# Kernel tuning notes

Measured on AMD Instinct MI355X. Metric: run time of the kernel, lower is better.

## Reference

```python
import jax, jax.numpy as jnp
import numpy as np

FILTER_SIZE = 7
SIGMA = 1.5
K1 = 0.01
K2 = 0.03
MAX_VAL = 1.0
CHANNEL = 1


def _gaussian_kernel3d(size, channel, sigma):
    coords = jnp.arange(size, dtype=jnp.float32) - (size - 1.0) / 2.0
    g = -(coords ** 2) / (2.0 * sigma ** 2)
    # grid[i,j,k] = g[j] + g[i] + g[k], matching torch view(1,-1,1)+view(-1,1,1)+view(1,1,-1)
    grid = g[None, :, None] + g[:, None, None] + g[None, None, :]
    grid = jax.nn.softmax(grid.reshape(-1))
    kernel = grid.reshape(1, 1, size, size, size)
    return jnp.broadcast_to(kernel, (channel, 1, size, size, size))


def _dwconv3d(x, kernel, channel):
    # depthwise (groups=channel) valid conv, NCDHW
    return jax.lax.conv_general_dilated(
        x, kernel, window_strides=(1, 1, 1), padding='VALID',
        dimension_numbers=('NCDHW', 'OIDHW', 'NCDHW'),
        feature_group_count=channel)


def setup_inputs() -> dict:
    key = jax.random.key(0)
    k1, k2 = jax.random.split(key)
    shape = (2, 1, 192, 192, 192)
    return {
        'input': jax.random.uniform(k1, shape, dtype=jnp.float32),
        'target': jax.random.uniform(k2, shape, dtype=jnp.float32),
    }


def reference(input, target):
    kernel = _gaussian_kernel3d(FILTER_SIZE, CHANNEL, SIGMA)
    c1 = (K1 * MAX_VAL) ** 2
    c2 = (K2 * MAX_VAL) ** 2
    mu1 = _dwconv3d(input, kernel, CHANNEL)
    mu2 = _dwconv3d(target, kernel, CHANNEL)
    mu1_sq = mu1 * mu1
    mu2_sq = mu2 * mu2
    mu1_mu2 = mu1 * mu2
    sigma1_sq = _dwconv3d(input * input, kernel, CHANNEL) - mu1_sq
    sigma2_sq = _dwconv3d(target * target, kernel, CHANNEL) - mu2_sq
    sigma12 = _dwconv3d(input * target, kernel, CHANNEL) - mu1_mu2
    v1 = 2.0 * sigma12 + c2
    v2 = sigma1_sq + sigma2_sq + c2
    ssim = (2.0 * mu1_mu2 + c1) * v1 / ((mu1_sq + mu2_sq + c1) * v2)
    return jnp.mean(ssim)  # reduction='mean'
```

## Files before the change

kernel.cpp:

```cpp
#include <hip/hip_runtime.h>
#include <utility>


#define DIMS 192
#define OD   186
#define VOL  (DIMS * DIMS * DIMS)
#define ZCH  62
#define XCH  27
#define NCHX 7
#define NP   (XCH + 6)
#define YT   8
#define YIN  14

#define ZP_P   15
#define ZP_F   (ZCH * ZP_P)
#define YP_F   576
#define YP_OFF (5 * ZP_F)
#define LDS_N  (YP_OFF + 5 * YP_F)

__global__ __launch_bounds__(256, 4)
void ssim3d_kernel(const float* __restrict__ X, const float* __restrict__ Y,
                   double* __restrict__ acc_out) {
    __shared__ float lds[LDS_N];
    __shared__ float wsum[4];
    const int tid = threadIdx.x;

    float w[7];
    {
        float s = 0.f;
        #pragma unroll
        for (int t = 0; t < 7; ++t) {
            float d = (float)t - 3.0f;
            w[t] = expf(-d * d / 4.5f);
            s += w[t];
        }
        #pragma unroll
        for (int t = 0; t < 7; ++t)
            w[t] = __uint_as_float(__builtin_amdgcn_readfirstlane(__float_as_uint(w[t] / s)));
    }

    const int z0 = blockIdx.x * ZCH;
    const int y0 = blockIdx.y * YT;
    const int cx = blockIdx.z % NCHX;
    const int n  = blockIdx.z / NCHX;
    const int x0 = cx * XCH;

    const float* Xb = X + (size_t)n * VOL;
    const float* Yb = Y + (size_t)n * VOL;

    const int zj = tid >> 4;
    const int zs = tid & 15;
    const bool zact = (zj < YIN);
    const int zc = z0 + zs * 4;
    const int gy = min(y0 + zj, DIMS - 1);
    const unsigned rowoff = (unsigned)gy * DIMS + (unsigned)zc;
    const bool ztail = (zc + 9 > DIMS - 1);

    const int wv = tid >> 6;
    const int ln = tid & 63;
    const int ybase = (310 * wv) >> 2;
    const int ycnt  = ((310 * (wv + 1)) >> 2) - ybase;

    const int aj = wv;
    const int ak = ln;
    const bool v1 = (ak < ZCH) && (y0 + aj < OD);
    const bool v2 = (ak < ZCH) && (y0 + aj + 4 < OD);
    const int xmax = OD + 6 - x0;

    float acc[7][10];
    #pragma unroll
    for (int q = 0; q < 7; ++q)
        #pragma unroll
        for (int m = 0; m < 10; ++m) acc[q][m] = 0.f;

    float lsum = 0.f;
    const float c1 = 1e-4f, c2 = 9e-4f;

    float pfx[10], pfy[10];

    auto loadX = [&](int xi) {
        if (!zact) return;
        int gx = min(x0 + xi, DIMS - 1);
        const float* p = Xb + (size_t)gx * (DIMS * DIMS) + rowoff;
        #pragma unroll
        for (int t = 0; t < 4; ++t) {
            float2 a = *(const float2*)(p + 2 * t);
            pfx[2 * t] = a.x; pfx[2 * t + 1] = a.y;
        }
        if (!ztail) {
            float2 a = *(const float2*)(p + 8);
            pfx[8] = a.x; pfx[9] = a.y;
        } else { pfx[8] = 0.f; pfx[9] = 0.f; }
    };
    auto loadY = [&](int xi) {
        if (!zact) return;
        int gx = min(x0 + xi, DIMS - 1);
        const float* p = Yb + (size_t)gx * (DIMS * DIMS) + rowoff;
        #pragma unroll
        for (int t = 0; t < 4; ++t) {
            float2 a = *(const float2*)(p + 2 * t);
            pfy[2 * t] = a.x; pfy[2 * t + 1] = a.y;
        }
        if (!ztail) {
            float2 a = *(const float2*)(p + 8);
            pfy[8] = a.x; pfy[9] = a.y;
        } else { pfy[8] = 0.f; pfy[9] = 0.f; }
    };

    auto ssim_pt = [&](float mu1, float mu2, float ex2, float ey2, float exy) {
        float mu11 = mu1 * mu1, mu22 = mu2 * mu2, mu12 = mu1 * mu2;
        float num = (2.f * mu12 + c1) * (2.f * (exy - mu12) + c2);
        float den = (mu11 + mu22 + c1) * ((ex2 - mu11) + (ey2 - mu22) + c2);
        lsum += num * __builtin_amdgcn_rcpf(den);
    };

    auto body = [&](int xi, auto ucell) {
        constexpr int U = decltype(ucell)::value;

        if (zact) {
            #pragma unroll
            for (int o = 0; o < 4; ++o) {
                float a0 = 0.f, a1 = 0.f, a2 = 0.f, a3 = 0.f, a4 = 0.f;
                #pragma unroll
                for (int t = 0; t < 7; ++t) {
                    float xx = pfx[o + t], yy = pfy[o + t], wt = w[t];
                    a0 += wt * xx;
                    a1 += wt * yy;
                    a2 += wt * (xx * xx);
                    a3 += wt * (yy * yy);
                    a4 += wt * (xx * yy);
                }
                int k = zs * 4 + o;
                if (k < ZCH) {
                    int b = k * ZP_P + zj;
                    lds[b]            = a0;
                    lds[b + ZP_F]     = a1;
                    lds[b + 2 * ZP_F] = a2;
                    lds[b + 3 * ZP_F] = a3;
                    lds[b + 4 * ZP_F] = a4;
                }
            }
        }
        if (xi + 1 < NP) loadX(xi + 1);
        __syncthreads();

        #pragma unroll
        for (int p2 = 0; p2 < 2; ++p2) {
            int rel = p2 * 64 + ln;
            if (rel < ycnt) {
                int t = ybase + rel;
                int f = t / ZCH;
                int k = t - f * ZCH;
                const float* src = &lds[f * ZP_F + k * ZP_P];
                float v[YIN];
                #pragma unroll
                for (int jj = 0; jj < YIN; ++jj) v[jj] = src[jj];
                float* dst = &lds[YP_OFF + f * YP_F + k * 9];
                #pragma unroll
                for (int j = 0; j < YT; ++j) {
                    float a = 0.f;
                    #pragma unroll
                    for (int tt = 0; tt < 7; ++tt) a += w[tt] * v[j + tt];
                    dst[j] = a;
                }
            }
        }
        if (xi + 1 < NP) loadY(xi + 1);
        __syncthreads();

        float vv[10];
        #pragma unroll
        for (int f = 0; f < 5; ++f) {
            vv[2 * f]     = lds[YP_OFF + f * YP_F + ak * 9 + aj];
            vv[2 * f + 1] = lds[YP_OFF + f * YP_F + ak * 9 + aj + 4];
        }
        #pragma unroll
        for (int d = 0; d < 7; ++d) {
            float wq = w[d];
            #pragma unroll
            for (int m = 0; m < 10; ++m)
                acc[(U + 7 - d) % 7][m] += wq * vv[m];
        }
        constexpr int sc = (U + 1) % 7;
        if (xi >= 6 && xi < xmax) {
            if (v1) ssim_pt(acc[sc][0], acc[sc][2], acc[sc][4], acc[sc][6], acc[sc][8]);
            if (v2) ssim_pt(acc[sc][1], acc[sc][3], acc[sc][5], acc[sc][7], acc[sc][9]);
        }
        #pragma unroll
        for (int m = 0; m < 10; ++m) acc[sc][m] = 0.f;
    };

    loadX(0); loadY(0);
    #pragma unroll 1
    for (int b = 0; b < 28; b += 7) {
        body(b + 0, std::integral_constant<int, 0>{});
        body(b + 1, std::integral_constant<int, 1>{});
        body(b + 2, std::integral_constant<int, 2>{});
        body(b + 3, std::integral_constant<int, 3>{});
        body(b + 4, std::integral_constant<int, 4>{});
        body(b + 5, std::integral_constant<int, 5>{});
        body(b + 6, std::integral_constant<int, 6>{});
    }
    body(28, std::integral_constant<int, 0>{});
    body(29, std::integral_constant<int, 1>{});
    body(30, std::integral_constant<int, 2>{});
    body(31, std::integral_constant<int, 3>{});
    body(32, std::integral_constant<int, 4>{});

    #pragma unroll
    for (int off = 32; off > 0; off >>= 1) lsum += __shfl_down(lsum, off, 64);
    if ((tid & 63) == 0) wsum[tid >> 6] = lsum;
    __syncthreads();
    if (tid == 0)
        atomicAdd(acc_out, (double)(wsum[0] + wsum[1] + wsum[2] + wsum[3]));
}

__global__ void ssim3d_finalize(const double* __restrict__ acc, float* __restrict__ out) {
    out[0] = (float)(acc[0] / 12869712.0);
}

extern "C" void kernel_launch(void* const* d_in, const int* in_sizes, int n_in,
                              void* d_out, int out_size, void* d_ws, size_t ws_size,
                              hipStream_t stream) {
    (void)in_sizes; (void)n_in; (void)out_size; (void)ws_size;
    const float* x = (const float*)d_in[0];
    const float* y = (const float*)d_in[1];
    float* out = (float*)d_out;
    double* acc = (double*)d_ws;
    hipMemsetAsync(d_ws, 0, sizeof(double), stream);
    dim3 grid(3, 24, NCHX * 2);
    ssim3d_kernel<<<grid, 256, 0, stream>>>(x, y, acc);
    ssim3d_finalize<<<1, 1, 0, stream>>>(acc, out);
}
```

Baseline: 235.8 us.

## Shrink z-tile to 32, double occupancy, remap blocks, fuse finalize via atomic counter

```diff
diff --git a/kernel.cpp b/kernel.cpp
--- a/kernel.cpp
+++ b/kernel.cpp
@@ -5,7 +5,8 @@
 #define DIMS 192
 #define OD   186
 #define VOL  (DIMS * DIMS * DIMS)
-#define ZCH  62
+#define ZCH  32
+#define NZT  6
 #define XCH  27
 #define NCHX 7
 #define NP   (XCH + 6)
@@ -14,13 +15,17 @@
 
 #define ZP_P   15
 #define ZP_F   (ZCH * ZP_P)
-#define YP_F   576
+#define YP_P   9
+#define YP_F   (ZCH * YP_P)
 #define YP_OFF (5 * ZP_F)
 #define LDS_N  (YP_OFF + 5 * YP_F)
 
-__global__ __launch_bounds__(256, 4)
+#define NBLK   (NZT * 24 * NCHX * 2)
+
+__global__ __launch_bounds__(256, 8)
 void ssim3d_kernel(const float* __restrict__ X, const float* __restrict__ Y,
-                   double* __restrict__ acc_out) {
+                   double* __restrict__ acc_out, unsigned* __restrict__ cnt,
+                   float* __restrict__ out) {
     __shared__ float lds[LDS_N];
     __shared__ float wsum[4];
     const int tid = threadIdx.x;
@@ -39,10 +44,17 @@
             w[t] = __uint_as_float(__builtin_amdgcn_readfirstlane(__float_as_uint(w[t] / s)));
     }
 
-    const int z0 = blockIdx.x * ZCH;
-    const int y0 = blockIdx.y * YT;
-    const int cx = blockIdx.z % NCHX;
-    const int n  = blockIdx.z / NCHX;
+    const int L  = blockIdx.x + NZT * (blockIdx.y + 24 * blockIdx.z);
+    const int v  = (L & 7) * (NBLK / 8) + (L >> 3);
+    const int cb = v / 144;
+    const int rem = v - cb * 144;
+    const int by  = rem % 24;
+    const int bz  = rem / 24;
+    const int cx  = cb % NCHX;
+    const int n   = cb / NCHX;
+
+    const int z0 = bz * ZCH;
+    const int y0 = by * YT;
     const int x0 = cx * XCH;
 
     const float* Xb = X + (size_t)n * VOL;
@@ -51,60 +63,66 @@
     const int zj = tid >> 4;
     const int zs = tid & 15;
     const bool zact = (zj < YIN);
-    const int zc = z0 + zs * 4;
+    const int zc = z0 + zs * 2;
     const int gy = min(y0 + zj, DIMS - 1);
     const unsigned rowoff = (unsigned)gy * DIMS + (unsigned)zc;
-    const bool ztail = (zc + 9 > DIMS - 1);
-
-    const int wv = tid >> 6;
-    const int ln = tid & 63;
-    const int ybase = (310 * wv) >> 2;
-    const int ycnt  = ((310 * (wv + 1)) >> 2) - ybase;
-
-    const int aj = wv;
-    const int ak = ln;
-    const bool v1 = (ak < ZCH) && (y0 + aj < OD);
-    const bool v2 = (ak < ZCH) && (y0 + aj + 4 < OD);
+    const bool ztail = (zc + 7 > DIMS - 1);
+
+    const int bfld = tid >> 5;
+    const int bk   = tid & 31;
+    const bool bact = (bfld < 5);
+
+    const int aj = tid >> 5;
+    const int ak = tid & 31;
+    const bool av = (z0 + ak < OD) && (y0 + aj < OD);
     const int xmax = OD + 6 - x0;
 
-    float acc[7][10];
+    float acc[7][5];
     #pragma unroll
     for (int q = 0; q < 7; ++q)
         #pragma unroll
-        for (int m = 0; m < 10; ++m) acc[q][m] = 0.f;
+        for (int m = 0; m < 5; ++m) acc[q][m] = 0.f;
 
     float lsum = 0.f;
     const float c1 = 1e-4f, c2 = 9e-4f;
 
-    float pfx[10], pfy[10];
+    float pfx[8], pfy[8];
 
     auto loadX = [&](int xi) {
         if (!zact) return;
         int gx = min(x0 + xi, DIMS - 1);
-        const float* p = Xb + (size_t)gx * (DIMS * DIMS) + rowoff;
-        #pragma unroll
-        for (int t = 0; t < 4; ++t) {
-            float2 a = *(const float2*)(p + 2 * t);
-            pfx[2 * t] = a.x; pfx[2 * t + 1] = a.y;
-        }
+        const float* p = Xb + (size_t)gx * (DIMS * DIMS);
         if (!ztail) {
-            float2 a = *(const float2*)(p + 8);
-            pfx[8] = a.x; pfx[9] = a.y;
-        } else { pfx[8] = 0.f; pfx[9] = 0.f; }
+            const float* q = p + rowoff;
+            #pragma unroll
+            for (int t = 0; t < 4; ++t) {
+                float2 a = *(const float2*)(q + 2 * t);
+                pfx[2 * t] = a.x; pfx[2 * t + 1] = a.y;
+            }
+        } else {
+            unsigned ro = (unsigned)gy * DIMS;
+            #pragma unroll
+            for (int j = 0; j < 8; ++j)
+                pfx[j] = p[ro + (unsigned)min(zc + j, DIMS - 1)];
+        }
     };
     auto loadY = [&](int xi) {
         if (!zact) return;
         int gx = min(x0 + xi, DIMS - 1);
-        const float* p = Yb + (size_t)gx * (DIMS * DIMS) + rowoff;
-        #pragma unroll
-        for (int t = 0; t < 4; ++t) {
-            float2 a = *(const float2*)(p + 2 * t);
-            pfy[2 * t] = a.x; pfy[2 * t + 1] = a.y;
-        }
+        const float* p = Yb + (size_t)gx * (DIMS * DIMS);
         if (!ztail) {
-            float2 a = *(const float2*)(p + 8);
-            pfy[8] = a.x; pfy[9] = a.y;
-        } else { pfy[8] = 0.f; pfy[9] = 0.f; }
+            const float* q = p + rowoff;
+            #pragma unroll
+            for (int t = 0; t < 4; ++t) {
+                float2 a = *(const float2*)(q + 2 * t);
+                pfy[2 * t] = a.x; pfy[2 * t + 1] = a.y;
+            }
+        } else {
+            unsigned ro = (unsigned)gy * DIMS;
+            #pragma unroll
+            for (int j = 0; j < 8; ++j)
+                pfy[j] = p[ro + (unsigned)min(zc + j, DIMS - 1)];
+        }
     };
 
     auto ssim_pt = [&](float mu1, float mu2, float ex2, float ey2, float exy) {
@@ -119,7 +137,7 @@
 
         if (zact) {
             #pragma unroll
-            for (int o = 0; o < 4; ++o) {
+            for (int o = 0; o < 2; ++o) {
                 float a0 = 0.f, a1 = 0.f, a2 = 0.f, a3 = 0.f, a4 = 0.f;
                 #pragma unroll
                 for (int t = 0; t < 7; ++t) {
@@ -130,64 +148,50 @@
                     a3 += wt * (yy * yy);
                     a4 += wt * (xx * yy);
                 }
-                int k = zs * 4 + o;
-                if (k < ZCH) {
-                    int b = k * ZP_P + zj;
-                    lds[b]            = a0;
-                    lds[b + ZP_F]     = a1;
-                    lds[b + 2 * ZP_F] = a2;
-                    lds[b + 3 * ZP_F] = a3;
-                    lds[b + 4 * ZP_F] = a4;
-                }
+                int b = (zs * 2 + o) * ZP_P + zj;
+                lds[b]            = a0;
+                lds[b + ZP_F]     = a1;
+                lds[b + 2 * ZP_F] = a2;
+                lds[b + 3 * ZP_F] = a3;
+                lds[b + 4 * ZP_F] = a4;
             }
         }
         if (xi + 1 < NP) loadX(xi + 1);
         __syncthreads();
 
-        #pragma unroll
-        for (int p2 = 0; p2 < 2; ++p2) {
-            int rel = p2 * 64 + ln;
-            if (rel < ycnt) {
-                int t = ybase + rel;
-                int f = t / ZCH;
-                int k = t - f * ZCH;
-                const float* src = &lds[f * ZP_F + k * ZP_P];
-                float v[YIN];
+        if (bact) {
+            const float* src = &lds[bfld * ZP_F + bk * ZP_P];
+            float vy[YIN];
+            #pragma unroll
+            for (int jj = 0; jj < YIN; ++jj) vy[jj] = src[jj];
+            float* dst = &lds[YP_OFF + bfld * YP_F + bk * YP_P];
+            #pragma unroll
+            for (int j = 0; j < YT; ++j) {
+                float a = 0.f;
                 #pragma unroll
-                for (int jj = 0; jj < YIN; ++jj) v[jj] = src[jj];
-                float* dst = &lds[YP_OFF + f * YP_F + k * 9];
-                #pragma unroll
-                for (int j = 0; j < YT; ++j) {
-                    float a = 0.f;
-                    #pragma unroll
-                    for (int tt = 0; tt < 7; ++tt) a += w[tt] * v[j + tt];
-                    dst[j] = a;
-                }
+                for (int tt = 0; tt < 7; ++tt) a += w[tt] * vy[j + tt];
+                dst[j] = a;
             }
         }
         if (xi + 1 < NP) loadY(xi + 1);
         __syncthreads();
 
-        float vv[10];
-        #pragma unroll
-        for (int f = 0; f < 5; ++f) {
-            vv[2 * f]     = lds[YP_OFF + f * YP_F + ak * 9 + aj];
-            vv[2 * f + 1] = lds[YP_OFF + f * YP_F + ak * 9 + aj + 4];
-        }
+        float vv[5];
+        #pragma unroll
+        for (int f = 0; f < 5; ++f)
+            vv[f] = lds[YP_OFF + f * YP_F + ak * YP_P + aj];
         #pragma unroll
         for (int d = 0; d < 7; ++d) {
             float wq = w[d];
             #pragma unroll
-            for (int m = 0; m < 10; ++m)
+            for (int m = 0; m < 5; ++m)
                 acc[(U + 7 - d) % 7][m] += wq * vv[m];
         }
         constexpr int sc = (U + 1) % 7;
-        if (xi >= 6 && xi < xmax) {
-            if (v1) ssim_pt(acc[sc][0], acc[sc][2], acc[sc][4], acc[sc][6], acc[sc][8]);
-            if (v2) ssim_pt(acc[sc][1], acc[sc][3], acc[sc][5], acc[sc][7], acc[sc][9]);
-        }
-        #pragma unroll
-        for (int m = 0; m < 10; ++m) acc[sc][m] = 0.f;
+        if (xi >= 6 && xi < xmax && av)
+            ssim_pt(acc[sc][0], acc[sc][1], acc[sc][2], acc[sc][3], acc[sc][4]);
+        #pragma unroll
+        for (int m = 0; m < 5; ++m) acc[sc][m] = 0.f;
     };
 
     loadX(0); loadY(0);
@@ -211,12 +215,16 @@
     for (int off = 32; off > 0; off >>= 1) lsum += __shfl_down(lsum, off, 64);
     if ((tid & 63) == 0) wsum[tid >> 6] = lsum;
     __syncthreads();
-    if (tid == 0)
-        atomicAdd(acc_out, (double)(wsum[0] + wsum[1] + wsum[2] + wsum[3]));
-}
-
-__global__ void ssim3d_finalize(const double* __restrict__ acc, float* __restrict__ out) {
-    out[0] = (float)(acc[0] / 12869712.0);
+    if (tid == 0) {
+        double bs = (double)(wsum[0] + wsum[1] + wsum[2] + wsum[3]);
+        atomicAdd(acc_out, bs);
+        __threadfence();
+        unsigned prev = atomicAdd(cnt, 1u);
+        if (prev == (unsigned)(NBLK - 1)) {
+            double tot = atomicAdd(acc_out, 0.0);
+            out[0] = (float)(tot / 12869712.0);
+        }
+    }
 }
 
 extern "C" void kernel_launch(void* const* d_in, const int* in_sizes, int n_in,
@@ -225,10 +233,9 @@
     (void)in_sizes; (void)n_in; (void)out_size; (void)ws_size;
     const float* x = (const float*)d_in[0];
     const float* y = (const float*)d_in[1];
-    float* out = (float*)d_out;
     double* acc = (double*)d_ws;
-    hipMemsetAsync(d_ws, 0, sizeof(double), stream);
-    dim3 grid(3, 24, NCHX * 2);
-    ssim3d_kernel<<<grid, 256, 0, stream>>>(x, y, acc);
-    ssim3d_finalize<<<1, 1, 0, stream>>>(acc, out);
+    unsigned* cnt = (unsigned*)((char*)d_ws + 8);
+    hipMemsetAsync(d_ws, 0, 16, stream);
+    dim3 grid(NZT, 24, NCHX * 2);
+    ssim3d_kernel<<<grid, 256, 0, stream>>>(x, y, acc, cnt, (float*)d_out);
 }
```

After: 805.3 us. +241.5%, slower.

## Fuse finalize into main kernel, remap block order, adjust launch bounds

Applied to the files above, without the earlier changes.

```diff
diff --git a/kernel.cpp b/kernel.cpp
--- a/kernel.cpp
+++ b/kernel.cpp
@@ -6,6 +6,7 @@
 #define OD   186
 #define VOL  (DIMS * DIMS * DIMS)
 #define ZCH  62
+#define NZT  3
 #define XCH  27
 #define NCHX 7
 #define NP   (XCH + 6)
@@ -18,9 +19,14 @@
 #define YP_OFF (5 * ZP_F)
 #define LDS_N  (YP_OFF + 5 * YP_F)
 
-__global__ __launch_bounds__(256, 4)
+#define NBLK   (NZT * 24 * NCHX * 2)
+
+#define AI __attribute__((always_inline))
+
+__global__ __launch_bounds__(256, 3)
 void ssim3d_kernel(const float* __restrict__ X, const float* __restrict__ Y,
-                   double* __restrict__ acc_out) {
+                   double* __restrict__ acc_out, unsigned* __restrict__ cnt,
+                   float* __restrict__ out) {
     __shared__ float lds[LDS_N];
     __shared__ float wsum[4];
     const int tid = threadIdx.x;
@@ -39,10 +45,17 @@
             w[t] = __uint_as_float(__builtin_amdgcn_readfirstlane(__float_as_uint(w[t] / s)));
     }
 
-    const int z0 = blockIdx.x * ZCH;
-    const int y0 = blockIdx.y * YT;
-    const int cx = blockIdx.z % NCHX;
-    const int n  = blockIdx.z / NCHX;
+    const int L  = blockIdx.x + NZT * (blockIdx.y + 24 * blockIdx.z);
+    const int v  = (L & 7) * (NBLK / 8) + (L >> 3);
+    const int cb = v / 72;
+    const int rem = v - cb * 72;
+    const int by  = rem % 24;
+    const int bz  = rem / 24;
+    const int cx  = cb % NCHX;
+    const int n   = cb / NCHX;
+
+    const int z0 = bz * ZCH;
+    const int y0 = by * YT;
     const int x0 = cx * XCH;
 
     const float* Xb = X + (size_t)n * VOL;
@@ -78,7 +91,7 @@
 
     float pfx[10], pfy[10];
 
-    auto loadX = [&](int xi) {
+    auto loadX = [&](int xi) AI {
         if (!zact) return;
         int gx = min(x0 + xi, DIMS - 1);
         const float* p = Xb + (size_t)gx * (DIMS * DIMS) + rowoff;
@@ -92,7 +105,7 @@
             pfx[8] = a.x; pfx[9] = a.y;
         } else { pfx[8] = 0.f; pfx[9] = 0.f; }
     };
-    auto loadY = [&](int xi) {
+    auto loadY = [&](int xi) AI {
         if (!zact) return;
         int gx = min(x0 + xi, DIMS - 1);
         const float* p = Yb + (size_t)gx * (DIMS * DIMS) + rowoff;
@@ -107,14 +120,14 @@
         } else { pfy[8] = 0.f; pfy[9] = 0.f; }
     };
 
-    auto ssim_pt = [&](float mu1, float mu2, float ex2, float ey2, float exy) {
+    auto ssim_pt = [&](float mu1, float mu2, float ex2, float ey2, float exy) AI {
         float mu11 = mu1 * mu1, mu22 = mu2 * mu2, mu12 = mu1 * mu2;
         float num = (2.f * mu12 + c1) * (2.f * (exy - mu12) + c2);
         float den = (mu11 + mu22 + c1) * ((ex2 - mu11) + (ey2 - mu22) + c2);
         lsum += num * __builtin_amdgcn_rcpf(den);
     };
 
-    auto body = [&](int xi, auto ucell) {
+    auto body = [&](int xi, auto ucell) AI {
         constexpr int U = decltype(ucell)::value;
 
         if (zact) {
@@ -152,15 +165,15 @@
                 int f = t / ZCH;
                 int k = t - f * ZCH;
                 const float* src = &lds[f * ZP_F + k * ZP_P];
-                float v[YIN];
+                float vy[YIN];
                 #pragma unroll
-                for (int jj = 0; jj < YIN; ++jj) v[jj] = src[jj];
+                for (int jj = 0; jj < YIN; ++jj) vy[jj] = src[jj];
                 float* dst = &lds[YP_OFF + f * YP_F + k * 9];
                 #pragma unroll
                 for (int j = 0; j < YT; ++j) {
                     float a = 0.f;
                     #pragma unroll
-                    for (int tt = 0; tt < 7; ++tt) a += w[tt] * v[j + tt];
+                    for (int tt = 0; tt < 7; ++tt) a += w[tt] * vy[j + tt];
                     dst[j] = a;
                 }
             }
@@ -211,12 +224,16 @@
     for (int off = 32; off > 0; off >>= 1) lsum += __shfl_down(lsum, off, 64);
     if ((tid & 63) == 0) wsum[tid >> 6] = lsum;
     __syncthreads();
-    if (tid == 0)
-        atomicAdd(acc_out, (double)(wsum[0] + wsum[1] + wsum[2] + wsum[3]));
-}
-
-__global__ void ssim3d_finalize(const double* __restrict__ acc, float* __restrict__ out) {
-    out[0] = (float)(acc[0] / 12869712.0);
+    if (tid == 0) {
+        double bs = (double)(wsum[0] + wsum[1] + wsum[2] + wsum[3]);
+        atomicAdd(acc_out, bs);
+        __threadfence();
+        unsigned prev = atomicAdd(cnt, 1u);
+        if (prev == (unsigned)(NBLK - 1)) {
+            double tot = atomicAdd(acc_out, 0.0);
+            out[0] = (float)(tot / 12869712.0);
+        }
+    }
 }
 
 extern "C" void kernel_launch(void* const* d_in, const int* in_sizes, int n_in,
@@ -225,10 +242,9 @@
     (void)in_sizes; (void)n_in; (void)out_size; (void)ws_size;
     const float* x = (const float*)d_in[0];
     const float* y = (const float*)d_in[1];
-    float* out = (float*)d_out;
     double* acc = (double*)d_ws;
-    hipMemsetAsync(d_ws, 0, sizeof(double), stream);
-    dim3 grid(3, 24, NCHX * 2);
-    ssim3d_kernel<<<grid, 256, 0, stream>>>(x, y, acc);
-    ssim3d_finalize<<<1, 1, 0, stream>>>(acc, out);
+    unsigned* cnt = (unsigned*)((char*)d_ws + 8);
+    hipMemsetAsync(d_ws, 0, 16, stream);
+    dim3 grid(NZT, 24, NCHX * 2);
+    ssim3d_kernel<<<grid, 256, 0, stream>>>(x, y, acc, cnt, (float*)d_out);
 }
```

Result: slower. 243.7 us (+3.4%).
